# Optimization experiments

Hardware: AMD Instinct MI355X
Metric: run time of the kernel (lower is better)

## Reference

```python
import jax, jax.numpy as jnp
import numpy as np

B, DX, DY, H = 512, 128, 128, 512


def setup_inputs() -> dict:
    key = jax.random.key(0)
    ks = jax.random.split(key, 5)
    x = jax.random.normal(ks[0], (B, DX), dtype=jnp.float32)
    y = jax.random.normal(ks[1], (B, DY), dtype=jnp.float32)
    # torch nn.Linear-style weights [out_features, in_features], small init scale
    W1 = jax.random.normal(ks[2], (H, DX + DY), dtype=jnp.float32) * 0.05
    b1 = jnp.zeros((H,), dtype=jnp.float32)
    W2 = jax.random.normal(ks[3], (H, H), dtype=jnp.float32) * 0.05
    b2 = jnp.zeros((H,), dtype=jnp.float32)
    W3 = jax.random.normal(ks[4], (1, H), dtype=jnp.float32) * 0.05
    b3 = jnp.zeros((1,), dtype=jnp.float32)
    return {"x": x, "y": y, "W1": W1, "b1": b1, "W2": W2, "b2": b2, "W3": W3, "b3": b3}


def reference(x, y, W1, b1, W2, b2, W3, b3):
    # Original: pair (row i, col j) of the *returned* (transposed) matrix is
    # f(concat(x[i], y[j])). We fuse the B^2 concat + first Linear into two
    # B x H matmuls broadcast-summed (mathematically identical).
    dimX = x.shape[1]
    hx = jnp.einsum("id,hd->ih", x, W1[:, :dimX])          # [B, H]
    hy = jnp.einsum("jd,hd->jh", y, W1[:, dimX:])          # [B, H]
    h = jax.nn.relu(hx[:, None, :] + hy[None, :, :] + b1)   # [B, B, H]
    h = jax.nn.relu(jnp.einsum("ijh,kh->ijk", h, W2) + b2)  # [B, B, H]
    out = jnp.einsum("ijh,h->ij", h, W3[0]) + b3[0]         # [B, B]
    return out
```

## Files before the change

kernel.cpp:

```cpp
#include <hip/hip_runtime.h>
#include <hip/hip_bf16.h>

#define Bn  512
#define DXn 128
#define Hn  512

using bf16x8 = __attribute__((ext_vector_type(8))) short;
using f32x4  = __attribute__((ext_vector_type(4))) float;

static __device__ __forceinline__ unsigned short f2bf(float f) {
    unsigned int u = __float_as_uint(f);
    u = (u + 0x7fffu + ((u >> 16) & 1u)) >> 16;
    return (unsigned short)u;
}

__global__ __launch_bounds__(256) void prep_h(
    const float* __restrict__ x, const float* __restrict__ y,
    const float* __restrict__ W1, const float* __restrict__ b1,
    float* __restrict__ hxb, float* __restrict__ hyv)
{
    const int which = blockIdx.z;
    const int i0 = blockIdx.y * 16;
    const int h0 = blockIdx.x * 16;
    const float* __restrict__ src = which ? y : x;
    float* __restrict__ dst = which ? hyv : hxb;
    const int off = which ? DXn : 0;

    __shared__ float xs[16][129];
    __shared__ float ws[16][129];
    const int tx = threadIdx.x, ty = threadIdx.y;
    const int t = ty * 16 + tx;
    {
        const int base = t * 8;
        const int r = base >> 7;
        const int c = base & 127;
        const float4 v0 = *(const float4*)(&src[(i0 + r) * DXn + c]);
        const float4 v1 = *(const float4*)(&src[(i0 + r) * DXn + c + 4]);
        xs[r][c + 0] = v0.x; xs[r][c + 1] = v0.y; xs[r][c + 2] = v0.z; xs[r][c + 3] = v0.w;
        xs[r][c + 4] = v1.x; xs[r][c + 5] = v1.y; xs[r][c + 6] = v1.z; xs[r][c + 7] = v1.w;
        const float4 w0 = *(const float4*)(&W1[(h0 + r) * (2 * DXn) + off + c]);
        const float4 w1 = *(const float4*)(&W1[(h0 + r) * (2 * DXn) + off + c + 4]);
        ws[r][c + 0] = w0.x; ws[r][c + 1] = w0.y; ws[r][c + 2] = w0.z; ws[r][c + 3] = w0.w;
        ws[r][c + 4] = w1.x; ws[r][c + 5] = w1.y; ws[r][c + 6] = w1.z; ws[r][c + 7] = w1.w;
    }
    __syncthreads();
    float acc = which ? 0.0f : b1[h0 + tx];
    #pragma unroll 8
    for (int c = 0; c < DXn; ++c)
        acc = fmaf(xs[ty][c], ws[tx][c], acc);
    dst[(i0 + ty) * Hn + (h0 + tx)] = acc;
}

__global__ __launch_bounds__(256) void prep_w2(
    const float* __restrict__ W2, unsigned short* __restrict__ w2s)
{
    const int T = blockIdx.x * 256 + threadIdx.x;
    const int l  = T & 63;
    const int hf = (T >> 6) & 15;
    const int kf = T >> 10;
    const int row = kf * 16 + (l & 15);
    const int col = hf * 32 + (l >> 4) * 8;
    const float* p = &W2[row * Hn + col];
    const float4 v0 = *(const float4*)p;
    const float4 v1 = *(const float4*)(p + 4);
    union { unsigned short us[8]; uint4 v; } pk;
    pk.us[0] = f2bf(v0.x); pk.us[1] = f2bf(v0.y); pk.us[2] = f2bf(v0.z); pk.us[3] = f2bf(v0.w);
    pk.us[4] = f2bf(v1.x); pk.us[5] = f2bf(v1.y); pk.us[6] = f2bf(v1.z); pk.us[7] = f2bf(v1.w);
    *(uint4*)(w2s + (size_t)T * 8) = pk.v;
}

__global__ __launch_bounds__(512) void critic_main(
    const float* __restrict__ hxb, const float* __restrict__ hyv,
    const unsigned short* __restrict__ w2s, const float* __restrict__ b2,
    const float* __restrict__ W3, const float* __restrict__ b3,
    float* __restrict__ out)
{
    __shared__ __align__(16) unsigned char smem[65536];
    unsigned short* a_lds = (unsigned short*)smem;
    float* red = (float*)smem;

    const int i   = blockIdx.y;
    const int j0  = blockIdx.x * 64;
    const int tid = threadIdx.x;
    const int w   = tid >> 6;
    const int l   = tid & 63;
    const int lg  = l >> 4;
    const int lm  = l & 15;

    {
        const int fr  = w & 3;
        const int fhb = (w >> 2) * 8;
        const int r   = fr * 16 + lm;
        const float* __restrict__ hyrow = &hyv[(size_t)(j0 + r) * Hn];
        const float* __restrict__ hxrow = &hxb[(size_t)i * Hn];
        #pragma unroll
        for (int q = 0; q < 8; ++q) {
            const int fh = fhb + q;
            const int h0 = fh * 32 + lg * 8;
            const float4 a0 = *(const float4*)(hyrow + h0);
            const float4 a1 = *(const float4*)(hyrow + h0 + 4);
            const float4 x0 = *(const float4*)(hxrow + h0);
            const float4 x1 = *(const float4*)(hxrow + h0 + 4);
            union { unsigned short us[8]; uint4 v; } pk;
            pk.us[0] = f2bf(fmaxf(a0.x + x0.x, 0.f));
            pk.us[1] = f2bf(fmaxf(a0.y + x0.y, 0.f));
            pk.us[2] = f2bf(fmaxf(a0.z + x0.z, 0.f));
            pk.us[3] = f2bf(fmaxf(a0.w + x0.w, 0.f));
            pk.us[4] = f2bf(fmaxf(a1.x + x1.x, 0.f));
            pk.us[5] = f2bf(fmaxf(a1.y + x1.y, 0.f));
            pk.us[6] = f2bf(fmaxf(a1.z + x1.z, 0.f));
            pk.us[7] = f2bf(fmaxf(a1.w + x1.w, 0.f));
            *(uint4*)(a_lds + ((size_t)(fr * 16 + fh) * 64 + l) * 8) = pk.v;
        }
    }
    __syncthreads();

    f32x4 acc[4][4] = {};
    const unsigned short* __restrict__ wbase =
        w2s + (size_t)(w * 4) * 16 * 64 * 8;

    #pragma unroll 4
    for (int s = 0; s < 16; ++s) {
        bf16x8 a[4], b[4];
        #pragma unroll
        for (int fi = 0; fi < 4; ++fi)
            a[fi] = *(const bf16x8*)(a_lds + ((size_t)(fi * 16 + s) * 64 + l) * 8);
        #pragma unroll
        for (int fj = 0; fj < 4; ++fj)
            b[fj] = *(const bf16x8*)(wbase + ((size_t)(fj * 16 + s) * 64 + l) * 8);
        #pragma unroll
        for (int fi = 0; fi < 4; ++fi)
            #pragma unroll
            for (int fj = 0; fj < 4; ++fj)
                acc[fi][fj] = __builtin_amdgcn_mfma_f32_16x16x32_bf16(
                    a[fi], b[fj], acc[fi][fj], 0, 0, 0);
    }

    float b2v[4], w3v[4];
    #pragma unroll
    for (int fj = 0; fj < 4; ++fj) {
        const int k = w * 64 + fj * 16 + lm;
        b2v[fj] = b2[k];
        w3v[fj] = W3[k];
    }
    float rp[4][4];
    #pragma unroll
    for (int fi = 0; fi < 4; ++fi) {
        #pragma unroll
        for (int q = 0; q < 4; ++q) {
            float ssum = 0.f;
            #pragma unroll
            for (int fj = 0; fj < 4; ++fj) {
                float c = acc[fi][fj][q] + b2v[fj];
                c = fmaxf(c, 0.f);
                ssum = fmaf(c, w3v[fj], ssum);
            }
            rp[fi][q] = ssum;
        }
    }
    #pragma unroll
    for (int m = 1; m < 16; m <<= 1) {
        #pragma unroll
        for (int fi = 0; fi < 4; ++fi)
            #pragma unroll
            for (int q = 0; q < 4; ++q)
                rp[fi][q] += __shfl_xor(rp[fi][q], m, 64);
    }

    __syncthreads();
    if (lm == 0) {
        #pragma unroll
        for (int fi = 0; fi < 4; ++fi)
            #pragma unroll
            for (int q = 0; q < 4; ++q)
                red[w * 64 + fi * 16 + lg * 4 + q] = rp[fi][q];
    }
    __syncthreads();
    if (tid < 64) {
        float ssum = 0.f;
        #pragma unroll
        for (int ww = 0; ww < 8; ++ww) ssum += red[ww * 64 + tid];
        out[(size_t)i * Bn + j0 + tid] = ssum + b3[0];
    }
}

extern "C" void kernel_launch(void* const* d_in, const int* in_sizes, int n_in,
                              void* d_out, int out_size, void* d_ws, size_t ws_size,
                              hipStream_t stream) {
    const float* x  = (const float*)d_in[0];
    const float* y  = (const float*)d_in[1];
    const float* W1 = (const float*)d_in[2];
    const float* b1 = (const float*)d_in[3];
    const float* W2 = (const float*)d_in[4];
    const float* b2 = (const float*)d_in[5];
    const float* W3 = (const float*)d_in[6];
    const float* b3 = (const float*)d_in[7];
    float* out = (float*)d_out;

    char* ws = (char*)d_ws;
    float* hxb = (float*)ws;
    float* hyv = (float*)(ws + (size_t)Bn * Hn * 4);
    unsigned short* w2s = (unsigned short*)(ws + (size_t)2 * Bn * Hn * 4);

    prep_h<<<dim3(Hn / 16, Bn / 16, 2), dim3(16, 16), 0, stream>>>(x, y, W1, b1, hxb, hyv);
    prep_w2<<<dim3(128), dim3(256), 0, stream>>>(W2, w2s);
    critic_main<<<dim3(Bn / 64, Bn), dim3(512), 0, stream>>>(hxb, hyv, w2s, b2, W3, b3, out);
}
```

Before: 243.5 us.

## Register-tile prep GEMM, double-buffer W2 fragment loads, use packed bf16 conversion

prep_h switches to a larger block tile: each thread computes 2x4 outputs using float4 LDS reads instead of one scalar dot product. The main kernel's K loop is fully unrolled and prefetches the next step's W2 B-fragments into a second register buffer while the MFMAs for the current step run. Manual bf16 rounding is replaced with the packed __float22bfloat162_rn intrinsic, and critic_main gains a min-blocks launch bound of 4. The aim is to hide global-load latency in the main loop and cut conversion ALU work, at the cost of higher register pressure under the tighter occupancy constraint.

```diff
diff --git a/kernel.cpp b/kernel.cpp
--- a/kernel.cpp
+++ b/kernel.cpp
@@ -8,10 +8,10 @@
 using bf16x8 = __attribute__((ext_vector_type(8))) short;
 using f32x4  = __attribute__((ext_vector_type(4))) float;
 
-static __device__ __forceinline__ unsigned short f2bf(float f) {
-    unsigned int u = __float_as_uint(f);
-    u = (u + 0x7fffu + ((u >> 16) & 1u)) >> 16;
-    return (unsigned short)u;
+static __device__ __forceinline__ unsigned int pkbf(float lo, float hi) {
+    union { __hip_bfloat162 b; unsigned int u; } cv;
+    cv.b = __float22bfloat162_rn(make_float2(lo, hi));
+    return cv.u;
 }
 
 __global__ __launch_bounds__(256) void prep_h(
@@ -20,35 +20,54 @@
     float* __restrict__ hxb, float* __restrict__ hyv)
 {
     const int which = blockIdx.z;
-    const int i0 = blockIdx.y * 16;
-    const int h0 = blockIdx.x * 16;
+    const int i0 = blockIdx.y * 32;
+    const int h0 = blockIdx.x * 64;
     const float* __restrict__ src = which ? y : x;
     float* __restrict__ dst = which ? hyv : hxb;
     const int off = which ? DXn : 0;
 
-    __shared__ float xs[16][129];
-    __shared__ float ws[16][129];
-    const int tx = threadIdx.x, ty = threadIdx.y;
-    const int t = ty * 16 + tx;
-    {
-        const int base = t * 8;
-        const int r = base >> 7;
-        const int c = base & 127;
-        const float4 v0 = *(const float4*)(&src[(i0 + r) * DXn + c]);
-        const float4 v1 = *(const float4*)(&src[(i0 + r) * DXn + c + 4]);
-        xs[r][c + 0] = v0.x; xs[r][c + 1] = v0.y; xs[r][c + 2] = v0.z; xs[r][c + 3] = v0.w;
-        xs[r][c + 4] = v1.x; xs[r][c + 5] = v1.y; xs[r][c + 6] = v1.z; xs[r][c + 7] = v1.w;
-        const float4 w0 = *(const float4*)(&W1[(h0 + r) * (2 * DXn) + off + c]);
-        const float4 w1 = *(const float4*)(&W1[(h0 + r) * (2 * DXn) + off + c + 4]);
-        ws[r][c + 0] = w0.x; ws[r][c + 1] = w0.y; ws[r][c + 2] = w0.z; ws[r][c + 3] = w0.w;
-        ws[r][c + 4] = w1.x; ws[r][c + 5] = w1.y; ws[r][c + 6] = w1.z; ws[r][c + 7] = w1.w;
-    }
-    __syncthreads();
-    float acc = which ? 0.0f : b1[h0 + tx];
-    #pragma unroll 8
-    for (int c = 0; c < DXn; ++c)
-        acc = fmaf(xs[ty][c], ws[tx][c], acc);
-    dst[(i0 + ty) * Hn + (h0 + tx)] = acc;
+    __shared__ float xs[32][132];
+    __shared__ float ws[64][132];
+    const int t = threadIdx.x;
+    #pragma unroll
+    for (int it = 0; it < 4; ++it) {
+        const int fi = it * 256 + t;
+        const int r = fi >> 5, q = fi & 31;
+        *(float4*)&xs[r][q * 4] = *(const float4*)&src[(i0 + r) * DXn + q * 4];
+    }
+    #pragma unroll
+    for (int it = 0; it < 8; ++it) {
+        const int fi = it * 256 + t;
+        const int r = fi >> 5, q = fi & 31;
+        *(float4*)&ws[r][q * 4] = *(const float4*)&W1[(h0 + r) * (2 * DXn) + off + q * 4];
+    }
+    __syncthreads();
+
+    const int tx = t & 15;
+    const int ty = t >> 4;
+    float acc[2][4];
+    #pragma unroll
+    for (int v = 0; v < 2; ++v)
+        #pragma unroll
+        for (int u = 0; u < 4; ++u)
+            acc[v][u] = which ? 0.0f : b1[h0 + tx + u * 16];
+
+    #pragma unroll 4
+    for (int c4 = 0; c4 < 32; ++c4) {
+        const float4 xv0 = *(const float4*)&xs[ty * 2 + 0][c4 * 4];
+        const float4 xv1 = *(const float4*)&xs[ty * 2 + 1][c4 * 4];
+        #pragma unroll
+        for (int u = 0; u < 4; ++u) {
+            const float4 wv = *(const float4*)&ws[tx + u * 16][c4 * 4];
+            acc[0][u] = fmaf(xv0.x, wv.x, fmaf(xv0.y, wv.y, fmaf(xv0.z, wv.z, fmaf(xv0.w, wv.w, acc[0][u]))));
+            acc[1][u] = fmaf(xv1.x, wv.x, fmaf(xv1.y, wv.y, fmaf(xv1.z, wv.z, fmaf(xv1.w, wv.w, acc[1][u]))));
+        }
+    }
+    #pragma unroll
+    for (int v = 0; v < 2; ++v)
+        #pragma unroll
+        for (int u = 0; u < 4; ++u)
+            dst[(size_t)(i0 + ty * 2 + v) * Hn + h0 + tx + u * 16] = acc[v][u];
 }
 
 __global__ __launch_bounds__(256) void prep_w2(
@@ -63,13 +82,15 @@
     const float* p = &W2[row * Hn + col];
     const float4 v0 = *(const float4*)p;
     const float4 v1 = *(const float4*)(p + 4);
-    union { unsigned short us[8]; uint4 v; } pk;
-    pk.us[0] = f2bf(v0.x); pk.us[1] = f2bf(v0.y); pk.us[2] = f2bf(v0.z); pk.us[3] = f2bf(v0.w);
-    pk.us[4] = f2bf(v1.x); pk.us[5] = f2bf(v1.y); pk.us[6] = f2bf(v1.z); pk.us[7] = f2bf(v1.w);
-    *(uint4*)(w2s + (size_t)T * 8) = pk.v;
-}
-
-__global__ __launch_bounds__(512) void critic_main(
+    uint4 pk;
+    pk.x = pkbf(v0.x, v0.y);
+    pk.y = pkbf(v0.z, v0.w);
+    pk.z = pkbf(v1.x, v1.y);
+    pk.w = pkbf(v1.z, v1.w);
+    *(uint4*)(w2s + (size_t)T * 8) = pk;
+}
+
+__global__ __launch_bounds__(512, 4) void critic_main(
     const float* __restrict__ hxb, const float* __restrict__ hyv,
     const unsigned short* __restrict__ w2s, const float* __restrict__ b2,
     const float* __restrict__ W3, const float* __restrict__ b3,
@@ -101,16 +122,12 @@
             const float4 a1 = *(const float4*)(hyrow + h0 + 4);
             const float4 x0 = *(const float4*)(hxrow + h0);
             const float4 x1 = *(const float4*)(hxrow + h0 + 4);
-            union { unsigned short us[8]; uint4 v; } pk;
-            pk.us[0] = f2bf(fmaxf(a0.x + x0.x, 0.f));
-            pk.us[1] = f2bf(fmaxf(a0.y + x0.y, 0.f));
-            pk.us[2] = f2bf(fmaxf(a0.z + x0.z, 0.f));
-            pk.us[3] = f2bf(fmaxf(a0.w + x0.w, 0.f));
-            pk.us[4] = f2bf(fmaxf(a1.x + x1.x, 0.f));
-            pk.us[5] = f2bf(fmaxf(a1.y + x1.y, 0.f));
-            pk.us[6] = f2bf(fmaxf(a1.z + x1.z, 0.f));
-            pk.us[7] = f2bf(fmaxf(a1.w + x1.w, 0.f));
-            *(uint4*)(a_lds + ((size_t)(fr * 16 + fh) * 64 + l) * 8) = pk.v;
+            uint4 pk;
+            pk.x = pkbf(fmaxf(a0.x + x0.x, 0.f), fmaxf(a0.y + x0.y, 0.f));
+            pk.y = pkbf(fmaxf(a0.z + x0.z, 0.f), fmaxf(a0.w + x0.w, 0.f));
+            pk.z = pkbf(fmaxf(a1.x + x1.x, 0.f), fmaxf(a1.y + x1.y, 0.f));
+            pk.w = pkbf(fmaxf(a1.z + x1.z, 0.f), fmaxf(a1.w + x1.w, 0.f));
+            *(uint4*)(a_lds + ((size_t)(fr * 16 + fh) * 64 + l) * 8) = pk;
         }
     }
     __syncthreads();
@@ -119,21 +136,29 @@
     const unsigned short* __restrict__ wbase =
         w2s + (size_t)(w * 4) * 16 * 64 * 8;
 
-    #pragma unroll 4
+    bf16x8 b[2][4];
+    #pragma unroll
+    for (int fj = 0; fj < 4; ++fj)
+        b[0][fj] = *(const bf16x8*)(wbase + ((size_t)(fj * 16) * 64 + l) * 8);
+
+    #pragma unroll
     for (int s = 0; s < 16; ++s) {
-        bf16x8 a[4], b[4];
+        const int cur = s & 1, nxt = cur ^ 1;
+        if (s < 15) {
+            #pragma unroll
+            for (int fj = 0; fj < 4; ++fj)
+                b[nxt][fj] = *(const bf16x8*)(wbase + ((size_t)(fj * 16 + s + 1) * 64 + l) * 8);
+        }
+        bf16x8 a[4];
         #pragma unroll
         for (int fi = 0; fi < 4; ++fi)
             a[fi] = *(const bf16x8*)(a_lds + ((size_t)(fi * 16 + s) * 64 + l) * 8);
-        #pragma unroll
-        for (int fj = 0; fj < 4; ++fj)
-            b[fj] = *(const bf16x8*)(wbase + ((size_t)(fj * 16 + s) * 64 + l) * 8);
         #pragma unroll
         for (int fi = 0; fi < 4; ++fi)
             #pragma unroll
             for (int fj = 0; fj < 4; ++fj)
                 acc[fi][fj] = __builtin_amdgcn_mfma_f32_16x16x32_bf16(
-                    a[fi], b[fj], acc[fi][fj], 0, 0, 0);
+                    a[fi], b[cur][fj], acc[fi][fj], 0, 0, 0);
     }
 
     float b2v[4], w3v[4];
@@ -202,7 +227,7 @@
     float* hyv = (float*)(ws + (size_t)Bn * Hn * 4);
     unsigned short* w2s = (unsigned short*)(ws + (size_t)2 * Bn * Hn * 4);
 
-    prep_h<<<dim3(Hn / 16, Bn / 16, 2), dim3(16, 16), 0, stream>>>(x, y, W1, b1, hxb, hyv);
+    prep_h<<<dim3(Hn / 64, Bn / 32, 2), dim3(256), 0, stream>>>(x, y, W1, b1, hxb, hyv);
     prep_w2<<<dim3(128), dim3(256), 0, stream>>>(W2, w2s);
     critic_main<<<dim3(Bn / 64, Bn), dim3(512), 0, stream>>>(hxb, hyv, w2s, b2, W3, b3, out);
 }
```

New measurement: 235.1 us. 1.04x faster.
